# Kernel optimization log

Measured on AMD Instinct MI355X. Metric: run time of the kernel, lower is better.

The kernel has to match this reference:

```python
import jax, jax.numpy as jnp
import numpy as np

IN_F = 2048
OUT_F = 2048
NNZ = 1048576
B = 8192


def setup_inputs() -> dict:
    key = jax.random.key(0)
    k1, k2, k3 = jax.random.split(key, 3)
    x = jax.random.normal(k1, (B, IN_F), dtype=jnp.float32)
    weights = (jax.random.normal(k2, (NNZ,), dtype=jnp.float32) * 0.02).astype(jnp.float16)
    coords = jax.random.randint(k3, (NNZ,), 0, OUT_F * IN_F, dtype=jnp.int64)
    return {"x": x, "weights": weights, "coords": coords}


def reference(x, weights, coords):
    # COO SpMV: out[b, row] += w * x[b, col] for each (row, col, w) triple.
    # coords are flat indices into the [OUT_F, IN_F] weight matrix.
    rows = coords // IN_F
    cols = coords % IN_F
    # Scatter-accumulate sparse weights into a dense matrix (duplicates add,
    # matching the kernel's atomic accumulation), then one batched matmul
    # replaces the per-row kernel launches of the original.
    W = jnp.zeros((OUT_F, IN_F), dtype=jnp.float32)
    W = W.at[rows, cols].add(weights.astype(jnp.float32))
    out = jnp.einsum('bi,oi->bo', x, W)  # [B, OUT_F] fp32, like the CL buffer
    return out.astype(x.dtype)
```

## Files before the change

kernel.cpp:

```cpp
#include <hip/hip_runtime.h>
#include <hip/hip_fp16.h>

#define IN_F   2048
#define OUT_F  2048
#define NNZ_   1048576
#define BATCH  8192
#define W_ROW0 6144
#define W_BASE ((size_t)W_ROW0 * OUT_F)

typedef __bf16 bf16x8 __attribute__((ext_vector_type(8)));
typedef float  f32x4  __attribute__((ext_vector_type(4)));

__device__ __forceinline__ float bfval(unsigned short b) {
    union { unsigned int u; float f; } t; t.u = ((unsigned int)b) << 16; return t.f;
}
__device__ __forceinline__ unsigned short f2bf(float f) {
    union { float f; unsigned int u; } v; v.f = f;
    unsigned int u = v.u; u += 0x7FFF + ((u >> 16) & 1);
    return (unsigned short)(u >> 16);
}
__device__ __forceinline__ float h2f(unsigned short b) {
    union { unsigned short u; __half h; } t; t.u = b; return __half2float(t.h);
}
__device__ __forceinline__ void gload_lds16(const void* g, void* l) {
    __builtin_amdgcn_global_load_lds(
        (const __attribute__((address_space(1))) unsigned int*)g,
        (__attribute__((address_space(3))) unsigned int*)l,
        16, 0, 0);
}

__global__ void zero_f32_kernel(float4* __restrict__ p, int n4) {
    int s = gridDim.x * blockDim.x;
    for (int i = blockIdx.x * blockDim.x + threadIdx.x; i < n4; i += s)
        p[i] = float4{0.f, 0.f, 0.f, 0.f};
}

__global__ void scatter_xcvt_kernel(const unsigned short* __restrict__ wbits,
                                    const int* __restrict__ coords,
                                    float* __restrict__ W,
                                    const float4* __restrict__ x,
                                    ushort4* __restrict__ xb) {
    if (blockIdx.x < 512) {
        __shared__ unsigned int sbf, sfh;
        if (threadIdx.x == 0) { sbf = 0u; sfh = 0u; }
        __syncthreads();
        unsigned int mbf = 0u, mfh = 0u;
        for (int i = threadIdx.x; i < 512; i += blockDim.x) {
            unsigned short b = wbits[i];
            unsigned int abf = (((unsigned int)b) << 16) & 0x7FFFFFFFu;
            unsigned int afh = (unsigned int)(b & 0x7FFF);
            mbf = mbf > abf ? mbf : abf;
            mfh = mfh > afh ? mfh : afh;
        }
        atomicMax(&sbf, mbf); atomicMax(&sfh, mfh);
        __syncthreads();
        union { unsigned int u; float f; } tb; tb.u = sbf;
        float bmax = tb.f;
        float hmax = h2f((unsigned short)sfh);
        int mode = (bmax > 1e-3f && bmax < 16.f) ? 0
                 : (hmax > 1e-3f && hmax < 16.f) ? 1 : 2;

        const int stride = 512 * 256;
#pragma unroll
        for (int it = 0; it < 8; ++it) {
            int i = it * stride + blockIdx.x * 256 + threadIdx.x;
            float v;
            if (mode == 0)      v = bfval(wbits[i]);
            else if (mode == 1) v = h2f(wbits[i]);
            else                v = ((const float*)wbits)[i];
            atomicAdd(&W[coords[i] & (OUT_F * IN_F - 1)], v);
        }
    } else {
        const int t0     = (blockIdx.x - 512) * 256 + threadIdx.x;
        const int stride = 1536 * 256;
        for (int i = t0; i < BATCH * IN_F / 4; i += stride) {
            float4 v = x[i];
            ushort4 o;
            o.x = f2bf(v.x); o.y = f2bf(v.y); o.z = f2bf(v.z); o.w = f2bf(v.w);
            xb[i] = o;
        }
    }
}

__global__ void f32_to_bf16_kernel(const float4* __restrict__ in,
                                   ushort4* __restrict__ out, int n4) {
    int s = gridDim.x * blockDim.x;
    for (int i = blockIdx.x * blockDim.x + threadIdx.x; i < n4; i += s) {
        float4 v = in[i];
        ushort4 o;
        o.x = f2bf(v.x); o.y = f2bf(v.y); o.z = f2bf(v.z); o.w = f2bf(v.w);
        out[i] = o;
    }
}

__global__ __launch_bounds__(1024, 4) void gemm256_kernel(
    const unsigned short* __restrict__ xb,
    const unsigned short* __restrict__ wb,
    float* __restrict__ out) {
    constexpr int K = IN_F;
    constexpr int NT = K / 64;

    __shared__ __align__(16) unsigned short As[2][256 * 64];
    __shared__ __align__(16) unsigned short Bs[2][256 * 64];

    const int tid  = threadIdx.x;
    const int lane = tid & 63;
    const int wave = tid >> 6;
    const int wr   = wave >> 2;
    const int wc   = wave & 3;
    const int frow = lane & 15;
    const int klan = lane >> 4;
    const int s0   = klan ^ (lane & 7);

    const int flat = blockIdx.x;
    const int swz  = (flat & 7) * 32 + (flat >> 3);
    const int tm   = swz & 31;
    const int tn   = swz >> 5;

    const unsigned short* srcA = xb + (size_t)tm * 256 * K;
    const unsigned short* srcB = wb + (size_t)tn * 256 * K;

    const int rloc  = lane >> 3;
    const int sslot = (lane & 7) ^ rloc;

    f32x4 acc[4][4] = {};

    auto stage = [&](int buf, int kt) {
        const size_t coff = (size_t)kt * 64 + sslot * 8;
#pragma unroll
        for (int c = 0; c < 2; ++c) {
            const int row = c * 128 + wave * 8;
            gload_lds16(srcA + (size_t)(row + rloc) * K + coff,
                        &As[buf][row * 64]);
        }
#pragma unroll
        for (int c = 0; c < 2; ++c) {
            const int row = c * 128 + wave * 8;
            gload_lds16(srcB + (size_t)(row + rloc) * K + coff,
                        &Bs[buf][row * 64]);
        }
    };

    auto compute = [&](int buf) {
#pragma unroll
        for (int ks = 0; ks < 2; ++ks) {
            const int sl = s0 ^ (ks * 4);
            bf16x8 af[4], bg[4];
#pragma unroll
            for (int mf = 0; mf < 4; ++mf)
                af[mf] = *(const bf16x8*)
                    &As[buf][(wr * 64 + mf * 16 + frow) * 64 + sl * 8];
#pragma unroll
            for (int nf = 0; nf < 4; ++nf)
                bg[nf] = *(const bf16x8*)
                    &Bs[buf][(wc * 64 + nf * 16 + frow) * 64 + sl * 8];
            __builtin_amdgcn_s_setprio(1);
#pragma unroll
            for (int mf = 0; mf < 4; ++mf)
#pragma unroll
                for (int nf = 0; nf < 4; ++nf)
                    acc[mf][nf] = __builtin_amdgcn_mfma_f32_16x16x32_bf16(
                        bg[nf], af[mf], acc[mf][nf], 0, 0, 0);
            __builtin_amdgcn_s_setprio(0);
        }
    };

    stage(0, 0);
    stage(1, 1);

    for (int kt = 0; kt < NT - 2; ++kt) {
        asm volatile("s_waitcnt vmcnt(4)" ::: "memory");
        __builtin_amdgcn_s_barrier();
        compute(kt & 1);
        asm volatile("" ::: "memory");
        __builtin_amdgcn_s_barrier();
        stage(kt & 1, kt + 2);
    }
    asm volatile("s_waitcnt vmcnt(4)" ::: "memory");
    __builtin_amdgcn_s_barrier();
    compute((NT - 2) & 1);
    asm volatile("" ::: "memory");
    __builtin_amdgcn_s_barrier();
    asm volatile("s_waitcnt vmcnt(0)" ::: "memory");
    __builtin_amdgcn_s_barrier();
    compute((NT - 1) & 1);

    const int orow0 = tm * 256 + wr * 64 + frow;
    const int ocol0 = tn * 256 + wc * 64 + klan * 4;
#pragma unroll
    for (int mf = 0; mf < 4; ++mf)
#pragma unroll
        for (int nf = 0; nf < 4; ++nf) {
            float4 v;
            v.x = acc[mf][nf][0]; v.y = acc[mf][nf][1];
            v.z = acc[mf][nf][2]; v.w = acc[mf][nf][3];
            *(float4*)&out[(size_t)(orow0 + mf * 16) * OUT_F
                           + ocol0 + nf * 16] = v;
        }
}

extern "C" void kernel_launch(void* const* d_in, const int* in_sizes, int n_in,
                              void* d_out, int out_size, void* d_ws, size_t ws_size,
                              hipStream_t stream) {
    const float*          x      = (const float*)d_in[0];
    const unsigned short* wbits  = (const unsigned short*)d_in[1];
    const int*            coords = (const int*)d_in[2];
    float*                out    = (float*)d_out;

    const size_t MB = 1024 * 1024;
    float*          W  = out + W_BASE;
    unsigned short* wb = (unsigned short*)d_ws;
    unsigned short* xb = (unsigned short*)((char*)d_ws + 8 * MB);
    (void)ws_size; (void)in_sizes; (void)n_in; (void)out_size;

    zero_f32_kernel<<<512, 256, 0, stream>>>((float4*)W, OUT_F * IN_F / 4);
    scatter_xcvt_kernel<<<2048, 256, 0, stream>>>(
        wbits, coords, W, (const float4*)x, (ushort4*)xb);
    f32_to_bf16_kernel<<<1024, 256, 0, stream>>>(
        (const float4*)W, (ushort4*)wb, OUT_F * IN_F / 4);

    gemm256_kernel<<<256, 1024, 0, stream>>>(xb, wb, out);
}
```

Measured before the change: 140.3 us.

## Replace global atomic scatter with counting-sort bucketing by row and LDS accumulation

```diff
diff --git a/kernel.cpp b/kernel.cpp
--- a/kernel.cpp
+++ b/kernel.cpp
@@ -5,18 +5,19 @@
 #define OUT_F  2048
 #define NNZ_   1048576
 #define BATCH  8192
-#define W_ROW0 6144
-#define W_BASE ((size_t)W_ROW0 * OUT_F)
+#define WMASK  (OUT_F * IN_F - 1)
+#define TAIL_F ((size_t)6144 * OUT_F)
 
 typedef __bf16 bf16x8 __attribute__((ext_vector_type(8)));
 typedef float  f32x4  __attribute__((ext_vector_type(4)));
+typedef unsigned int u32;
 
 __device__ __forceinline__ float bfval(unsigned short b) {
-    union { unsigned int u; float f; } t; t.u = ((unsigned int)b) << 16; return t.f;
+    union { u32 u; float f; } t; t.u = ((u32)b) << 16; return t.f;
 }
 __device__ __forceinline__ unsigned short f2bf(float f) {
-    union { float f; unsigned int u; } v; v.f = f;
-    unsigned int u = v.u; u += 0x7FFF + ((u >> 16) & 1);
+    union { float f; u32 u; } v; v.f = f;
+    u32 u = v.u; u += 0x7FFF + ((u >> 16) & 1);
     return (unsigned short)(u >> 16);
 }
 __device__ __forceinline__ float h2f(unsigned short b) {
@@ -29,49 +30,25 @@
         16, 0, 0);
 }
 
-__global__ void zero_f32_kernel(float4* __restrict__ p, int n4) {
-    int s = gridDim.x * blockDim.x;
-    for (int i = blockIdx.x * blockDim.x + threadIdx.x; i < n4; i += s)
-        p[i] = float4{0.f, 0.f, 0.f, 0.f};
-}
-
-__global__ void scatter_xcvt_kernel(const unsigned short* __restrict__ wbits,
-                                    const int* __restrict__ coords,
-                                    float* __restrict__ W,
-                                    const float4* __restrict__ x,
-                                    ushort4* __restrict__ xb) {
-    if (blockIdx.x < 512) {
-        __shared__ unsigned int sbf, sfh;
-        if (threadIdx.x == 0) { sbf = 0u; sfh = 0u; }
+__global__ void hist_xcvt_kernel(const int* __restrict__ coords,
+                                 u32* __restrict__ gh,
+                                 const float4* __restrict__ x,
+                                 ushort4* __restrict__ xb) {
+    if (blockIdx.x < 256) {
+        __shared__ u32 lbin[2048];
+        for (int i = threadIdx.x; i < 2048; i += 256) lbin[i] = 0u;
         __syncthreads();
-        unsigned int mbf = 0u, mfh = 0u;
-        for (int i = threadIdx.x; i < 512; i += blockDim.x) {
-            unsigned short b = wbits[i];
-            unsigned int abf = (((unsigned int)b) << 16) & 0x7FFFFFFFu;
-            unsigned int afh = (unsigned int)(b & 0x7FFF);
-            mbf = mbf > abf ? mbf : abf;
-            mfh = mfh > afh ? mfh : afh;
-        }
-        atomicMax(&sbf, mbf); atomicMax(&sfh, mfh);
+        const int base = blockIdx.x * 4096;
+#pragma unroll
+        for (int j = 0; j < 16; ++j) {
+            int c = coords[base + j * 256 + threadIdx.x] & WMASK;
+            atomicAdd(&lbin[c >> 11], 1u);
+        }
         __syncthreads();
-        union { unsigned int u; float f; } tb; tb.u = sbf;
-        float bmax = tb.f;
-        float hmax = h2f((unsigned short)sfh);
-        int mode = (bmax > 1e-3f && bmax < 16.f) ? 0
-                 : (hmax > 1e-3f && hmax < 16.f) ? 1 : 2;
-
-        const int stride = 512 * 256;
-#pragma unroll
-        for (int it = 0; it < 8; ++it) {
-            int i = it * stride + blockIdx.x * 256 + threadIdx.x;
-            float v;
-            if (mode == 0)      v = bfval(wbits[i]);
-            else if (mode == 1) v = h2f(wbits[i]);
-            else                v = ((const float*)wbits)[i];
-            atomicAdd(&W[coords[i] & (OUT_F * IN_F - 1)], v);
-        }
+        for (int r = threadIdx.x; r < 2048; r += 256)
+            gh[r * 256 + blockIdx.x] = lbin[r];
     } else {
-        const int t0     = (blockIdx.x - 512) * 256 + threadIdx.x;
+        const int t0     = (blockIdx.x - 256) * 256 + threadIdx.x;
         const int stride = 1536 * 256;
         for (int i = t0; i < BATCH * IN_F / 4; i += stride) {
             float4 v = x[i];
@@ -82,14 +59,109 @@
     }
 }
 
-__global__ void f32_to_bf16_kernel(const float4* __restrict__ in,
-                                   ushort4* __restrict__ out, int n4) {
-    int s = gridDim.x * blockDim.x;
-    for (int i = blockIdx.x * blockDim.x + threadIdx.x; i < n4; i += s) {
-        float4 v = in[i];
+__global__ void scanA_kernel(u32* __restrict__ gh, u32* __restrict__ rt) {
+    const int r = blockIdx.x * 256 + threadIdx.x;
+    u32 run = 0;
+    for (int b = 0; b < 256; ++b) {
+        u32 t = gh[r * 256 + b];
+        gh[r * 256 + b] = run;
+        run += t;
+    }
+    rt[r] = run;
+}
+
+__global__ void scanB_kernel(const u32* __restrict__ rt, u32* __restrict__ rb) {
+    __shared__ u32 s[2048];
+    __shared__ u32 part[256];
+    const int tid = threadIdx.x;
+    for (int i = tid; i < 2048; i += 256) s[i] = rt[i];
+    __syncthreads();
+    u32 sum = 0;
+#pragma unroll
+    for (int j = 0; j < 8; ++j) sum += s[tid * 8 + j];
+    part[tid] = sum;
+    __syncthreads();
+    if (tid == 0) {
+        u32 run = 0;
+        for (int i = 0; i < 256; ++i) { u32 t = part[i]; part[i] = run; run += t; }
+    }
+    __syncthreads();
+    u32 run = part[tid];
+#pragma unroll
+    for (int j = 0; j < 8; ++j) { u32 t = s[tid * 8 + j]; s[tid * 8 + j] = run; run += t; }
+    __syncthreads();
+    for (int i = tid; i < 2048; i += 256) rb[i] = s[i];
+    if (tid == 0) rb[2048] = NNZ_;
+}
+
+__global__ void place_kernel(const unsigned short* __restrict__ wbits,
+                             const int* __restrict__ coords,
+                             const u32* __restrict__ gh, const u32* __restrict__ rb,
+                             unsigned short* __restrict__ cs, float* __restrict__ wsr) {
+    __shared__ u32 cnt[2048];
+    __shared__ u32 sbf, sfh;
+    if (threadIdx.x == 0) { sbf = 0u; sfh = 0u; }
+    __syncthreads();
+    u32 mbf = 0u, mfh = 0u;
+    for (int i = threadIdx.x; i < 512; i += 256) {
+        unsigned short b = wbits[i];
+        u32 abf = (((u32)b) << 16) & 0x7FFFFFFFu;
+        u32 afh = (u32)(b & 0x7FFF);
+        mbf = mbf > abf ? mbf : abf;
+        mfh = mfh > afh ? mfh : afh;
+    }
+    atomicMax(&sbf, mbf); atomicMax(&sfh, mfh);
+    __syncthreads();
+    union { u32 u; float f; } tb; tb.u = sbf;
+    float bmax = tb.f;
+    float hmax = h2f((unsigned short)sfh);
+    const int mode = (bmax > 1e-3f && bmax < 16.f) ? 0
+                   : (hmax > 1e-3f && hmax < 16.f) ? 1 : 2;
+
+    for (int r = threadIdx.x; r < 2048; r += 256)
+        cnt[r] = rb[r] + gh[r * 256 + blockIdx.x];
+    __syncthreads();
+
+    const int base = blockIdx.x * 4096;
+#pragma unroll
+    for (int j = 0; j < 16; ++j) {
+        int i = base + j * 256 + threadIdx.x;
+        int c = coords[i] & WMASK;
+        int row = c >> 11, col = c & 2047;
+        float v;
+        if (mode == 0)      v = bfval(wbits[i]);
+        else if (mode == 1) v = h2f(wbits[i]);
+        else                v = ((const float*)wbits)[i];
+        u32 pos = atomicAdd(&cnt[row], 1u);
+        cs[pos]  = (unsigned short)col;
+        wsr[pos] = v;
+    }
+}
+
+__global__ void accum_kernel(const u32* __restrict__ rb,
+                             const unsigned short* __restrict__ cs,
+                             const float* __restrict__ wsr,
+                             ushort4* __restrict__ wb4) {
+    __shared__ float lacc[8 * 2048];
+    const int tid = threadIdx.x;
+    for (int i = tid; i < 16384; i += 256) lacc[i] = 0.f;
+    __syncthreads();
+#pragma unroll
+    for (int j = 0; j < 8; ++j) {
+        const int row = blockIdx.x * 8 + j;
+        const u32 e = rb[row + 1];
+        for (u32 i = rb[row] + tid; i < e; i += 256)
+            atomicAdd(&lacc[j * 2048 + cs[i]], wsr[i]);
+    }
+    __syncthreads();
+#pragma unroll
+    for (int k = 0; k < 16; ++k) {
+        const int e4 = k * 256 + tid;
+        const int e  = e4 * 4;
         ushort4 o;
-        o.x = f2bf(v.x); o.y = f2bf(v.y); o.z = f2bf(v.z); o.w = f2bf(v.w);
-        out[i] = o;
+        o.x = f2bf(lacc[e]);     o.y = f2bf(lacc[e + 1]);
+        o.z = f2bf(lacc[e + 2]); o.w = f2bf(lacc[e + 3]);
+        wb4[(size_t)blockIdx.x * 4096 + e4] = o;
     }
 }
 
@@ -208,16 +280,21 @@
     float*                out    = (float*)d_out;
 
     const size_t MB = 1024 * 1024;
-    float*          W  = out + W_BASE;
     unsigned short* wb = (unsigned short*)d_ws;
     unsigned short* xb = (unsigned short*)((char*)d_ws + 8 * MB);
+    u32*            gh  = (u32*)(out + TAIL_F);
+    u32*            rt  = gh + 2048 * 256;
+    u32*            rb  = rt + 2048;
+    unsigned short* cs  = (unsigned short*)((char*)(out + TAIL_F) + 4 * MB);
+    float*          wsr = (float*)((char*)(out + TAIL_F) + 8 * MB);
     (void)ws_size; (void)in_sizes; (void)n_in; (void)out_size;
 
-    zero_f32_kernel<<<512, 256, 0, stream>>>((float4*)W, OUT_F * IN_F / 4);
-    scatter_xcvt_kernel<<<2048, 256, 0, stream>>>(
-        wbits, coords, W, (const float4*)x, (ushort4*)xb);
-    f32_to_bf16_kernel<<<1024, 256, 0, stream>>>(
-        (const float4*)W, (ushort4*)wb, OUT_F * IN_F / 4);
+    hist_xcvt_kernel<<<1792, 256, 0, stream>>>(coords, gh, (const float4*)x,
+                                               (ushort4*)xb);
+    scanA_kernel<<<8, 256, 0, stream>>>(gh, rt);
+    scanB_kernel<<<1, 256, 0, stream>>>(rt, rb);
+    place_kernel<<<256, 256, 0, stream>>>(wbits, coords, gh, rb, cs, wsr);
+    accum_kernel<<<256, 256, 0, stream>>>(rb, cs, wsr, (ushort4*)wb);
 
     gemm256_kernel<<<256, 1024, 0, stream>>>(xb, wb, out);
 }
```

Result: slower. 157.7 us, median of 2 (+12.4%).

## Restructure GEMM to 8 waves with 4-phase interleaved load/MFMA pipeline

Applied to the files above, without the earlier changes.

```diff
diff --git a/kernel.cpp b/kernel.cpp
--- a/kernel.cpp
+++ b/kernel.cpp
@@ -10,6 +10,8 @@
 
 typedef __bf16 bf16x8 __attribute__((ext_vector_type(8)));
 typedef float  f32x4  __attribute__((ext_vector_type(4)));
+
+template <int N> struct ic { static constexpr int v = N; };
 
 __device__ __forceinline__ float bfval(unsigned short b) {
     union { unsigned int u; float f; } t; t.u = ((unsigned int)b) << 16; return t.f;
@@ -93,7 +95,7 @@
     }
 }
 
-__global__ __launch_bounds__(1024, 4) void gemm256_kernel(
+__global__ __launch_bounds__(512, 2) void gemm256_kernel(
     const unsigned short* __restrict__ xb,
     const unsigned short* __restrict__ wb,
     float* __restrict__ out) {
@@ -123,72 +125,88 @@
     const int rloc  = lane >> 3;
     const int sslot = (lane & 7) ^ rloc;
 
-    f32x4 acc[4][4] = {};
-
-    auto stage = [&](int buf, int kt) {
-        const size_t coff = (size_t)kt * 64 + sslot * 8;
-#pragma unroll
-        for (int c = 0; c < 2; ++c) {
-            const int row = c * 128 + wave * 8;
-            gload_lds16(srcA + (size_t)(row + rloc) * K + coff,
-                        &As[buf][row * 64]);
-        }
-#pragma unroll
-        for (int c = 0; c < 2; ++c) {
-            const int row = c * 128 + wave * 8;
-            gload_lds16(srcB + (size_t)(row + rloc) * K + coff,
-                        &Bs[buf][row * 64]);
-        }
+    f32x4 acc[8][4] = {};
+
+    auto stageA = [&](int buf, int kt, int chunk) {
+        const int row = chunk * 64 + wave * 8;
+        gload_lds16(srcA + (size_t)(row + rloc) * K + (size_t)kt * 64 + sslot * 8,
+                    &As[buf][row * 64]);
     };
-
-    auto compute = [&](int buf) {
-#pragma unroll
-        for (int ks = 0; ks < 2; ++ks) {
-            const int sl = s0 ^ (ks * 4);
-            bf16x8 af[4], bg[4];
-#pragma unroll
-            for (int mf = 0; mf < 4; ++mf)
-                af[mf] = *(const bf16x8*)
-                    &As[buf][(wr * 64 + mf * 16 + frow) * 64 + sl * 8];
-#pragma unroll
-            for (int nf = 0; nf < 4; ++nf)
-                bg[nf] = *(const bf16x8*)
-                    &Bs[buf][(wc * 64 + nf * 16 + frow) * 64 + sl * 8];
+    auto stageB = [&](int buf, int kt, int chunk) {
+        const int row = chunk * 64 + wave * 8;
+        gload_lds16(srcB + (size_t)(row + rloc) * K + (size_t)kt * 64 + sslot * 8,
+                    &Bs[buf][row * 64]);
+    };
+
+#pragma unroll
+    for (int c = 0; c < 4; ++c) stageB(0, 0, c);
+    stageA(0, 0, 0); stageA(0, 0, 2); stageA(0, 0, 1); stageA(0, 0, 3);
+#pragma unroll
+    for (int c = 0; c < 4; ++c) stageB(1, 1, c);
+    stageA(1, 1, 0); stageA(1, 1, 2);
+    asm volatile("s_waitcnt vmcnt(6)" ::: "memory");
+    __builtin_amdgcn_s_barrier();
+
+    for (int kt = 0; kt < NT; ++kt) {
+        const int b = kt & 1;
+
+        bf16x8 bg[4][2];
+#pragma unroll
+        for (int nf = 0; nf < 4; ++nf)
+#pragma unroll
+            for (int ks = 0; ks < 2; ++ks)
+                bg[nf][ks] = *(const bf16x8*)
+                    &Bs[b][(wc * 64 + nf * 16 + frow) * 64 + (s0 ^ (ks * 4)) * 8];
+
+        auto qphase = [&](auto MF0C, int stagesel) {
+            constexpr int MF0 = decltype(MF0C)::v;
+            bf16x8 af[2][2];
+#pragma unroll
+            for (int i = 0; i < 2; ++i)
+#pragma unroll
+                for (int ks = 0; ks < 2; ++ks)
+                    af[i][ks] = *(const bf16x8*)
+                        &As[b][(wr * 128 + (MF0 + i) * 16 + frow) * 64
+                               + (s0 ^ (ks * 4)) * 8];
+            if (stagesel == 0) {
+                if (kt + 1 < NT) { stageA(b ^ 1, kt + 1, 1); stageA(b ^ 1, kt + 1, 3); }
+            } else if (stagesel == 1) {
+                if (kt + 2 < NT) { stageB(b, kt + 2, 0); stageB(b, kt + 2, 1); }
+            } else if (stagesel == 2) {
+                if (kt + 2 < NT) { stageB(b, kt + 2, 2); stageB(b, kt + 2, 3); }
+            } else {
+                if (kt + 2 < NT) {
+                    stageA(b, kt + 2, 0); stageA(b, kt + 2, 2);
+                    asm volatile("s_waitcnt vmcnt(6)" ::: "memory");
+                } else if (kt + 1 < NT) {
+                    asm volatile("s_waitcnt vmcnt(0)" ::: "memory");
+                }
+            }
+            __builtin_amdgcn_s_barrier();
+            asm volatile("s_waitcnt lgkmcnt(0)" ::: "memory");
             __builtin_amdgcn_s_setprio(1);
 #pragma unroll
-            for (int mf = 0; mf < 4; ++mf)
+            for (int i = 0; i < 2; ++i)
 #pragma unroll
                 for (int nf = 0; nf < 4; ++nf)
-                    acc[mf][nf] = __builtin_amdgcn_mfma_f32_16x16x32_bf16(
-                        bg[nf], af[mf], acc[mf][nf], 0, 0, 0);
+#pragma unroll
+                    for (int ks = 0; ks < 2; ++ks)
+                        acc[MF0 + i][nf] = __builtin_amdgcn_mfma_f32_16x16x32_bf16(
+                            bg[nf][ks], af[i][ks], acc[MF0 + i][nf], 0, 0, 0);
             __builtin_amdgcn_s_setprio(0);
-        }
-    };
-
-    stage(0, 0);
-    stage(1, 1);
-
-    for (int kt = 0; kt < NT - 2; ++kt) {
-        asm volatile("s_waitcnt vmcnt(4)" ::: "memory");
-        __builtin_amdgcn_s_barrier();
-        compute(kt & 1);
-        asm volatile("" ::: "memory");
-        __builtin_amdgcn_s_barrier();
-        stage(kt & 1, kt + 2);
+            __builtin_amdgcn_s_barrier();
+        };
+
+        qphase(ic<0>{}, 0);
+        qphase(ic<2>{}, 1);
+        qphase(ic<4>{}, 2);
+        qphase(ic<6>{}, 3);
     }
-    asm volatile("s_waitcnt vmcnt(4)" ::: "memory");
-    __builtin_amdgcn_s_barrier();
-    compute((NT - 2) & 1);
-    asm volatile("" ::: "memory");
-    __builtin_amdgcn_s_barrier();
-    asm volatile("s_waitcnt vmcnt(0)" ::: "memory");
-    __builtin_amdgcn_s_barrier();
-    compute((NT - 1) & 1);
-
-    const int orow0 = tm * 256 + wr * 64 + frow;
+
+    const int orow0 = tm * 256 + wr * 128 + frow;
     const int ocol0 = tn * 256 + wc * 64 + klan * 4;
 #pragma unroll
-    for (int mf = 0; mf < 4; ++mf)
+    for (int mf = 0; mf < 8; ++mf)
 #pragma unroll
         for (int nf = 0; nf < 4; ++nf) {
             float4 v;
@@ -219,5 +237,5 @@
     f32_to_bf16_kernel<<<1024, 256, 0, stream>>>(
         (const float4*)W, (ushort4*)wb, OUT_F * IN_F / 4);
 
-    gemm256_kernel<<<256, 1024, 0, stream>>>(xb, wb, out);
-}
+    gemm256_kernel<<<256, 512, 0, stream>>>(xb, wb, out);
+}
```

Measured after the change: 154.1 us. +9.8%, slower.
